# Optimization experiments

Hardware: AMD Instinct MI355X
Metric: run time of the kernel (lower is better)

Reference implementation:

```python
import jax, jax.numpy as jnp
import numpy as np

N_NODES = 50000
N_EDGES = 800000
D = 128
NEG_SLOPE = 0.2
L2_EPS = 1e-12  # torch F.normalize eps


def setup_inputs() -> dict:
    key = jax.random.key(0)
    k1, k2, k3, k4, k5 = jax.random.split(key, 5)
    node_fts = jax.random.normal(k1, (N_NODES, D), dtype=jnp.float32)
    edges = jax.random.randint(k2, (2, N_EDGES), 0, N_NODES, dtype=jnp.int32)
    edge_fts = jax.random.normal(k3, (N_EDGES, 1), dtype=jnp.float32)
    # xavier-ish init for linear weights (stored as [out, in], matching nn.Linear)
    scale = 1.414 * np.sqrt(2.0 / (D + D))
    W_self = jax.random.normal(k4, (D, D), dtype=jnp.float32) * scale
    W_neigh = jax.random.normal(k5, (D, D), dtype=jnp.float32) * scale
    return {"node_fts": node_fts, "edges": edges, "edge_fts": edge_fts,
            "W_self": W_self, "W_neigh": W_neigh}


def reference(node_fts, edges, edge_fts, W_self, W_neigh):
    n = node_fts.shape[0]
    dst_idx = edges[0]  # segment ids (aggregation targets)
    src_idx = edges[1]  # gather ids (neighbor features)

    # self transform: [N, D]
    src_node_fts = node_fts @ W_self.T

    # gather neighbor feats along edges: [E, D]
    gathered = node_fts[src_idx]

    # scatter-mean into destination nodes
    seg_sum = jax.ops.segment_sum(gathered, dst_idx, num_segments=n)  # [N, D]
    cnt = jax.ops.segment_sum(jnp.ones((gathered.shape[0], 1), dtype=node_fts.dtype),
                              dst_idx, num_segments=n)                # [N, 1]
    neigh_mean = seg_sum / jnp.maximum(cnt, 1.0)

    # linear + LeakyReLU(0.2) on aggregated neighbors
    neigh_final = jax.nn.leaky_relu(neigh_mean @ W_neigh.T, NEG_SLOPE)

    # update: sum + LeakyReLU(0.2)
    updated = jax.nn.leaky_relu(src_node_fts + neigh_final, NEG_SLOPE)

    # L2 normalize per row (torch F.normalize semantics)
    norm = jnp.linalg.norm(updated, axis=1, keepdims=True)
    return updated / jnp.maximum(norm, L2_EPS)
```

## Files before the change

kernel.cpp:

```cpp
#include <hip/hip_runtime.h>
#include <hip/hip_bf16.h>

#define N_NODES 50000
#define N_EDGES 800000
#define D 128
#define NEG 0.2f

#define NB 200
#define EPB 4000
#define NPAIR 12500
#define NCH 8
#define ROWS_PER_CH 25

#define MFMA_BLOCKS 768
#define NTILES 3125
#define COLA_BLOCKS 391
#define FILL_SLICES 1600
#define FILL_EPS 500

typedef __attribute__((ext_vector_type(8))) short bf16x8;
typedef __attribute__((ext_vector_type(4))) float f32x4;

__device__ __forceinline__ float bflo(unsigned int u) {
    return __uint_as_float(u << 16);
}
__device__ __forceinline__ float bfhi(unsigned int u) {
    return __uint_as_float(u & 0xffff0000u);
}

__global__ __launch_bounds__(256) void hist_convert_kernel(
    const int* __restrict__ dst_idx,
    unsigned int* __restrict__ bh,
    unsigned char* __restrict__ rank8,
    const float4* __restrict__ ws4, const float4* __restrict__ wn4,
    ushort4* __restrict__ wb4) {
    __shared__ unsigned int lh[NPAIR];
    const int tid = threadIdx.x, b = blockIdx.x;
    if (b < NB) {
        for (int i = tid; i < NPAIR; i += 256) lh[i] = 0u;
        __syncthreads();
        const int e0 = b * EPB;
        for (int i = tid; i < EPB; i += 256) {
            int d = dst_idx[e0 + i];
            int sh = (d & 3) * 8;
            unsigned int old = atomicAdd(&lh[d >> 2], 1u << sh);
            rank8[e0 + i] = (unsigned char)((old >> sh) & 0xffu);
        }
        __syncthreads();
        for (int i = tid; i < NPAIR; i += 256) bh[(size_t)b * NPAIR + i] = lh[i];
    } else {
        int i = (b - NB) * 256 + tid;
        const int NW = D * D / 4;
        if (i < 2 * NW) {
            float4 v = (i < NW) ? ws4[i] : wn4[i - NW];
            ushort4 o;
            __hip_bfloat16 h;
            h = __float2bfloat16(v.x); o.x = reinterpret_cast<unsigned short&>(h);
            h = __float2bfloat16(v.y); o.y = reinterpret_cast<unsigned short&>(h);
            h = __float2bfloat16(v.z); o.z = reinterpret_cast<unsigned short&>(h);
            h = __float2bfloat16(v.w); o.w = reinterpret_cast<unsigned short&>(h);
            wb4[i] = o;
        }
    }
}

__global__ __launch_bounds__(256) void mfma_colA_kernel(
    const float* __restrict__ x, const ushort* __restrict__ wb,
    unsigned int* __restrict__ sb32, unsigned int* __restrict__ zb32,
    const unsigned int* __restrict__ bh, unsigned int* __restrict__ csum) {
    __shared__ ushort tile[2][16][132];
    if (blockIdx.x < MFMA_BLOCKS) {
        const int lane = threadIdx.x & 63;
        const int wv = threadIdx.x >> 6;
        const int lm = lane & 15;
        const int lk = (lane >> 4) * 8;
        const int dr = (lane >> 4) * 4;

        bf16x8 b[4][4];
#pragma unroll
        for (int t4 = 0; t4 < 4; ++t4) {
            const int nt = wv * 4 + t4;
#pragma unroll
            for (int kc = 0; kc < 4; ++kc)
                b[t4][kc] = *(const bf16x8*)(wb + (nt * 16 + lm) * D + kc * 32 + lk);
        }

        for (int t = blockIdx.x; t < NTILES; t += MFMA_BLOCKS) {
            const int m0 = t * 16;

            bf16x8 a[4];
#pragma unroll
            for (int kc = 0; kc < 4; ++kc) {
                const float* src = x + (long)(m0 + lm) * D + kc * 32 + lk;
                float4 f0 = *(const float4*)(src);
                float4 f1 = *(const float4*)(src + 4);
                bf16x8 af;
                __hip_bfloat16 h;
                h = __float2bfloat16(f0.x); af[0] = reinterpret_cast<short&>(h);
                h = __float2bfloat16(f0.y); af[1] = reinterpret_cast<short&>(h);
                h = __float2bfloat16(f0.z); af[2] = reinterpret_cast<short&>(h);
                h = __float2bfloat16(f0.w); af[3] = reinterpret_cast<short&>(h);
                h = __float2bfloat16(f1.x); af[4] = reinterpret_cast<short&>(h);
                h = __float2bfloat16(f1.y); af[5] = reinterpret_cast<short&>(h);
                h = __float2bfloat16(f1.z); af[6] = reinterpret_cast<short&>(h);
                h = __float2bfloat16(f1.w); af[7] = reinterpret_cast<short&>(h);
                a[kc] = af;
            }

#pragma unroll
            for (int t4 = 0; t4 < 4; ++t4) {
                const int nt = wv * 4 + t4;
                f32x4 acc = {0.f, 0.f, 0.f, 0.f};
#pragma unroll
                for (int kc = 0; kc < 4; ++kc)
                    acc = __builtin_amdgcn_mfma_f32_16x16x32_bf16(a[kc], b[t4][kc], acc, 0, 0, 0);
                ushort (*tptr)[132] = (nt < 8) ? tile[0] : tile[1];
                const int col = (nt & 7) * 16 + lm;
#pragma unroll
                for (int r = 0; r < 4; ++r) {
                    __hip_bfloat16 h = __float2bfloat16(acc[r]);
                    tptr[dr + r][col] = reinterpret_cast<unsigned short&>(h);
                }
            }
            __syncthreads();
            const unsigned int* ts32 = (const unsigned int*)tile[0];
            const unsigned int* tz32 = (const unsigned int*)tile[1];
#pragma unroll
            for (int q = 0; q < 4; ++q) {
                const int r16 = wv * 4 + q;
                sb32[(m0 + r16) * 64 + lane] = ts32[r16 * 66 + lane];
                zb32[(m0 + r16) * 64 + lane] = tz32[r16 * 66 + lane];
            }
            __syncthreads();
        }
    } else {
        int gid = (blockIdx.x - MFMA_BLOCKS) * 256 + threadIdx.x;
        if (gid >= NCH * NPAIR) return;
        int c = gid / NPAIR;
        int i = gid - c * NPAIR;
        const unsigned int* col = bh + (size_t)(c * ROWS_PER_CH) * NPAIR + i;
        unsigned int s = 0u;
#pragma unroll
        for (int r = 0; r < ROWS_PER_CH; ++r) s += col[(size_t)r * NPAIR];
        csum[c * NPAIR + i] = s;
    }
}

__global__ __launch_bounds__(1024) void colscanb_scan_kernel(
    unsigned int* __restrict__ bh, const unsigned int* __restrict__ csum,
    int* __restrict__ offs) {
    const int tid = threadIdx.x;
    if (blockIdx.x < 98) {
        int gid = blockIdx.x * 1024 + tid;
        if (gid >= NCH * NPAIR) return;
        int c = gid / NPAIR;
        int i = gid - c * NPAIR;
        unsigned int run = 0u;
        for (int cc = 0; cc < c; ++cc) run += csum[cc * NPAIR + i];
        unsigned int* col = bh + (size_t)(c * ROWS_PER_CH) * NPAIR + i;
#pragma unroll
        for (int r = 0; r < ROWS_PER_CH; ++r) {
            unsigned int v = col[(size_t)r * NPAIR];
            col[(size_t)r * NPAIR] = run;
            run += v;
        }
        return;
    }
    __shared__ int wsum[16];
    __shared__ int carry_s;
    const int lane = tid & 63, wv = tid >> 6;
    if (tid == 0) { carry_s = 0; offs[N_NODES] = N_EDGES; }
    __syncthreads();
    for (int base = 0; base < NPAIR; base += 4096) {
        int i0 = base + tid * 4;
        unsigned int p0 = 0, p1 = 0, p2 = 0, p3 = 0;
#pragma unroll
        for (int j = 0; j < 4; ++j) {
            int qi = i0 + j;
            if (qi < NPAIR) {
                unsigned int s = 0;
#pragma unroll
                for (int c = 0; c < NCH; ++c) s += csum[c * NPAIR + qi];
                if (j == 0) p0 = s; else if (j == 1) p1 = s;
                else if (j == 2) p2 = s; else p3 = s;
            }
        }
        int q0 = (int)((p0 & 0xffu) + ((p0 >> 8) & 0xffu) + ((p0 >> 16) & 0xffu) + (p0 >> 24));
        int q1 = (int)((p1 & 0xffu) + ((p1 >> 8) & 0xffu) + ((p1 >> 16) & 0xffu) + (p1 >> 24));
        int q2 = (int)((p2 & 0xffu) + ((p2 >> 8) & 0xffu) + ((p2 >> 16) & 0xffu) + (p2 >> 24));
        int q3 = (int)((p3 & 0xffu) + ((p3 >> 8) & 0xffu) + ((p3 >> 16) & 0xffu) + (p3 >> 24));
        int tsum = q0 + q1 + q2 + q3;
        int xs = tsum;
#pragma unroll
        for (int off = 1; off < 64; off <<= 1) {
            int y = __shfl_up(xs, off);
            if (lane >= off) xs += y;
        }
        if (lane == 63) wsum[wv] = xs;
        __syncthreads();
        if (wv == 0 && lane < 16) {
            int s = wsum[lane];
#pragma unroll
            for (int off = 1; off < 16; off <<= 1) {
                int y = __shfl_up(s, off);
                if (lane >= off) s += y;
            }
            wsum[lane] = s;
        }
        __syncthreads();
        int waveoff = (wv == 0) ? 0 : wsum[wv - 1];
        int excl = carry_s + waveoff + xs - tsum;
        unsigned int pk[4] = {p0, p1, p2, p3};
        int qs[4] = {q0, q1, q2, q3};
        int qbase = excl;
#pragma unroll
        for (int j = 0; j < 4; ++j) {
            int qi = i0 + j;
            if (qi < NPAIR) {
                unsigned int p = pk[j];
                int d0 = (int)(p & 0xffu), d1 = (int)((p >> 8) & 0xffu);
                int d2 = (int)((p >> 16) & 0xffu);
                int4 o; o.x = qbase; o.y = o.x + d0; o.z = o.y + d1; o.w = o.z + d2;
                *(int4*)(offs + 4 * qi) = o;
            }
            qbase += qs[j];
        }
        int total = wsum[15];
        __syncthreads();
        if (tid == 0) carry_s += total;
        __syncthreads();
    }
}

__global__ __launch_bounds__(256) void fill_kernel(
    const int* __restrict__ dst_idx, const int* __restrict__ src_idx,
    const unsigned char* __restrict__ rank8,
    const unsigned char* __restrict__ bprefix,
    const int* __restrict__ offs, unsigned short* __restrict__ adj) {
    const int e0 = blockIdx.x * FILL_EPS;
    const int b = e0 / EPB;
    const unsigned char* bp = bprefix + (size_t)b * N_NODES;
    for (int i = threadIdx.x; i < FILL_EPS; i += 256) {
        int e = e0 + i;
        int d = dst_idx[e];
        int pos = offs[d] + (int)bp[d] + (int)rank8[e];
        adj[pos] = (unsigned short)src_idx[e];
    }
}

__global__ __launch_bounds__(256) void gather_final_kernel(
    const uint4* __restrict__ zb4, const uint4* __restrict__ sb4,
    const int* __restrict__ offs,
    const unsigned short* __restrict__ adj, float4* __restrict__ out4) {
    int wid = (int)((blockIdx.x * (long)blockDim.x + threadIdx.x) >> 6);
    int lane = threadIdx.x & 63;
    if (wid >= N_NODES) return;
    const int c = lane & 15, g = lane >> 4;
    int base = offs[wid];
    int len = offs[wid + 1] - base;

    float a0 = 0.f, a1 = 0.f, a2 = 0.f, a3 = 0.f;
    float a4 = 0.f, a5 = 0.f, a6 = 0.f, a7 = 0.f;

    int k = 0;
    for (; k + 8 <= len; k += 8) {
        unsigned int sA = adj[base + k + g];
        unsigned int sB = adj[base + k + 4 + g];
        uint4 vA = zb4[sA * 16u + c];
        uint4 vB = zb4[sB * 16u + c];
        a0 += bflo(vA.x); a1 += bfhi(vA.x);
        a2 += bflo(vA.y); a3 += bfhi(vA.y);
        a4 += bflo(vA.z); a5 += bfhi(vA.z);
        a6 += bflo(vA.w); a7 += bfhi(vA.w);
        a0 += bflo(vB.x); a1 += bfhi(vB.x);
        a2 += bflo(vB.y); a3 += bfhi(vB.y);
        a4 += bflo(vB.z); a5 += bfhi(vB.z);
        a6 += bflo(vB.w); a7 += bfhi(vB.w);
    }
    if (k + 4 <= len) {
        unsigned int sA = adj[base + k + g];
        uint4 vA = zb4[sA * 16u + c];
        a0 += bflo(vA.x); a1 += bfhi(vA.x);
        a2 += bflo(vA.y); a3 += bfhi(vA.y);
        a4 += bflo(vA.z); a5 += bfhi(vA.z);
        a6 += bflo(vA.w); a7 += bfhi(vA.w);
        k += 4;
    }
    int rem = len - k;
    if (g < rem) {
        unsigned int sA = adj[base + k + g];
        uint4 vA = zb4[sA * 16u + c];
        a0 += bflo(vA.x); a1 += bfhi(vA.x);
        a2 += bflo(vA.y); a3 += bfhi(vA.y);
        a4 += bflo(vA.z); a5 += bfhi(vA.z);
        a6 += bflo(vA.w); a7 += bfhi(vA.w);
    }

    a0 += __shfl_xor(a0, 16); a1 += __shfl_xor(a1, 16);
    a2 += __shfl_xor(a2, 16); a3 += __shfl_xor(a3, 16);
    a4 += __shfl_xor(a4, 16); a5 += __shfl_xor(a5, 16);
    a6 += __shfl_xor(a6, 16); a7 += __shfl_xor(a7, 16);
    a0 += __shfl_xor(a0, 32); a1 += __shfl_xor(a1, 32);
    a2 += __shfl_xor(a2, 32); a3 += __shfl_xor(a3, 32);
    a4 += __shfl_xor(a4, 32); a5 += __shfl_xor(a5, 32);
    a6 += __shfl_xor(a6, 32); a7 += __shfl_xor(a7, 32);

    float inv = 1.0f / fmaxf((float)len, 1.0f);
    float m0 = a0 * inv, m1 = a1 * inv, m2 = a2 * inv, m3 = a3 * inv;
    float m4 = a4 * inv, m5 = a5 * inv, m6 = a6 * inv, m7 = a7 * inv;
    m0 = m0 > 0.f ? m0 : NEG * m0; m1 = m1 > 0.f ? m1 : NEG * m1;
    m2 = m2 > 0.f ? m2 : NEG * m2; m3 = m3 > 0.f ? m3 : NEG * m3;
    m4 = m4 > 0.f ? m4 : NEG * m4; m5 = m5 > 0.f ? m5 : NEG * m5;
    m6 = m6 > 0.f ? m6 : NEG * m6; m7 = m7 > 0.f ? m7 : NEG * m7;

    uint4 sv = sb4[(unsigned int)wid * 16u + c];
    float u0 = bflo(sv.x) + m0, u1 = bfhi(sv.x) + m1;
    float u2 = bflo(sv.y) + m2, u3 = bfhi(sv.y) + m3;
    float u4 = bflo(sv.z) + m4, u5 = bfhi(sv.z) + m5;
    float u6 = bflo(sv.w) + m6, u7 = bfhi(sv.w) + m7;
    u0 = u0 > 0.f ? u0 : NEG * u0; u1 = u1 > 0.f ? u1 : NEG * u1;
    u2 = u2 > 0.f ? u2 : NEG * u2; u3 = u3 > 0.f ? u3 : NEG * u3;
    u4 = u4 > 0.f ? u4 : NEG * u4; u5 = u5 > 0.f ? u5 : NEG * u5;
    u6 = u6 > 0.f ? u6 : NEG * u6; u7 = u7 > 0.f ? u7 : NEG * u7;

    float ss = u0 * u0 + u1 * u1 + u2 * u2 + u3 * u3 +
               u4 * u4 + u5 * u5 + u6 * u6 + u7 * u7;
    ss += __shfl_xor(ss, 1);
    ss += __shfl_xor(ss, 2);
    ss += __shfl_xor(ss, 4);
    ss += __shfl_xor(ss, 8);
    float r = 1.0f / fmaxf(sqrtf(ss), 1e-12f);

    if (lane < 16) {
        float4 o0; o0.x = u0 * r; o0.y = u1 * r; o0.z = u2 * r; o0.w = u3 * r;
        float4 o1; o1.x = u4 * r; o1.y = u5 * r; o1.z = u6 * r; o1.w = u7 * r;
        out4[(unsigned int)wid * 32u + c * 2u] = o0;
        out4[(unsigned int)wid * 32u + c * 2u + 1u] = o1;
    }
}

extern "C" void kernel_launch(void* const* d_in, const int* in_sizes, int n_in,
                              void* d_out, int out_size, void* d_ws, size_t ws_size,
                              hipStream_t stream) {
    const float* node_fts = (const float*)d_in[0];
    const int* edges = (const int*)d_in[1];
    const float* W_self = (const float*)d_in[3];
    const float* W_neigh = (const float*)d_in[4];

    const int* dst_idx = edges;
    const int* src_idx = edges + N_EDGES;

    unsigned short* zb = (unsigned short*)d_ws;
    unsigned short* sb = zb + (size_t)N_NODES * D;
    unsigned short* wb = sb + (size_t)N_NODES * D;
    int* offs = (int*)(wb + 256 * 128);
    unsigned short* adj = (unsigned short*)(offs + N_NODES + 1);
    unsigned int* bh = (unsigned int*)(adj + N_EDGES);
    unsigned char* rank8 = (unsigned char*)(bh + (size_t)NB * NPAIR);
    unsigned int* csum = (unsigned int*)(rank8 + N_EDGES);

    hist_convert_kernel<<<NB + 32, 256, 0, stream>>>(
        dst_idx, bh, rank8,
        (const float4*)W_self, (const float4*)W_neigh, (ushort4*)wb);

    mfma_colA_kernel<<<MFMA_BLOCKS + COLA_BLOCKS, 256, 0, stream>>>(
        node_fts, wb, (unsigned int*)sb, (unsigned int*)zb, bh, csum);

    colscanb_scan_kernel<<<99, 1024, 0, stream>>>(bh, csum, offs);

    fill_kernel<<<FILL_SLICES, 256, 0, stream>>>(
        dst_idx, src_idx, rank8, (const unsigned char*)bh, offs, adj);

    int gb = (N_NODES * 64 + 255) / 256;
    gather_final_kernel<<<gb, 256, 0, stream>>>(
        (const uint4*)zb, (const uint4*)sb, offs, adj, (float4*)d_out);
}
```

Baseline: 106.3 us.

## Fuse weight conversion and MFMA transform into histogram kernel, split colA out

The histogram blocks and the MFMA dense-transform blocks now run in one launch. MFMA blocks convert the fp32 weights to bf16 in registers directly, so the separate bf16 weight buffer is gone. The column-sum pass moves into its own small kernel because it depends on the histogram results. This lets the transform overlap the histogram phase instead of running after it. In exchange, the kernel reserves the larger 50KB shared histogram for every block, which may lower occupancy for the MFMA blocks, and each MFMA block reloads the weights as fp32.

```diff
diff --git a/kernel.cpp b/kernel.cpp
--- a/kernel.cpp
+++ b/kernel.cpp
@@ -28,15 +28,31 @@
     return __uint_as_float(u & 0xffff0000u);
 }
 
-__global__ __launch_bounds__(256) void hist_convert_kernel(
+__device__ __forceinline__ bf16x8 cvt8(const float4& f0, const float4& f1) {
+    bf16x8 af;
+    __hip_bfloat16 h;
+    h = __float2bfloat16(f0.x); af[0] = reinterpret_cast<short&>(h);
+    h = __float2bfloat16(f0.y); af[1] = reinterpret_cast<short&>(h);
+    h = __float2bfloat16(f0.z); af[2] = reinterpret_cast<short&>(h);
+    h = __float2bfloat16(f0.w); af[3] = reinterpret_cast<short&>(h);
+    h = __float2bfloat16(f1.x); af[4] = reinterpret_cast<short&>(h);
+    h = __float2bfloat16(f1.y); af[5] = reinterpret_cast<short&>(h);
+    h = __float2bfloat16(f1.z); af[6] = reinterpret_cast<short&>(h);
+    h = __float2bfloat16(f1.w); af[7] = reinterpret_cast<short&>(h);
+    return af;
+}
+
+__global__ __launch_bounds__(256) void hist_mfma_kernel(
     const int* __restrict__ dst_idx,
     unsigned int* __restrict__ bh,
     unsigned char* __restrict__ rank8,
-    const float4* __restrict__ ws4, const float4* __restrict__ wn4,
-    ushort4* __restrict__ wb4) {
-    __shared__ unsigned int lh[NPAIR];
+    const float* __restrict__ Ws, const float* __restrict__ Wn,
+    const float* __restrict__ x,
+    unsigned int* __restrict__ sb32, unsigned int* __restrict__ zb32) {
+    __shared__ unsigned int smem[NPAIR];
     const int tid = threadIdx.x, b = blockIdx.x;
     if (b < NB) {
+        unsigned int* lh = smem;
         for (int i = tid; i < NPAIR; i += 256) lh[i] = 0u;
         __syncthreads();
         const int e0 = b * EPB;
@@ -49,43 +65,30 @@
         __syncthreads();
         for (int i = tid; i < NPAIR; i += 256) bh[(size_t)b * NPAIR + i] = lh[i];
     } else {
-        int i = (b - NB) * 256 + tid;
-        const int NW = D * D / 4;
-        if (i < 2 * NW) {
-            float4 v = (i < NW) ? ws4[i] : wn4[i - NW];
-            ushort4 o;
-            __hip_bfloat16 h;
-            h = __float2bfloat16(v.x); o.x = reinterpret_cast<unsigned short&>(h);
-            h = __float2bfloat16(v.y); o.y = reinterpret_cast<unsigned short&>(h);
-            h = __float2bfloat16(v.z); o.z = reinterpret_cast<unsigned short&>(h);
-            h = __float2bfloat16(v.w); o.w = reinterpret_cast<unsigned short&>(h);
-            wb4[i] = o;
-        }
-    }
-}
-
-__global__ __launch_bounds__(256) void mfma_colA_kernel(
-    const float* __restrict__ x, const ushort* __restrict__ wb,
-    unsigned int* __restrict__ sb32, unsigned int* __restrict__ zb32,
-    const unsigned int* __restrict__ bh, unsigned int* __restrict__ csum) {
-    __shared__ ushort tile[2][16][132];
-    if (blockIdx.x < MFMA_BLOCKS) {
         const int lane = threadIdx.x & 63;
         const int wv = threadIdx.x >> 6;
         const int lm = lane & 15;
         const int lk = (lane >> 4) * 8;
         const int dr = (lane >> 4) * 4;
-
-        bf16x8 b[4][4];
+        ushort (*tile0)[132] = (ushort (*)[132])smem;
+        ushort (*tile1)[132] = ((ushort (*)[132])smem) + 16;
+
+        bf16x8 bfr[4][4];
 #pragma unroll
         for (int t4 = 0; t4 < 4; ++t4) {
             const int nt = wv * 4 + t4;
-#pragma unroll
-            for (int kc = 0; kc < 4; ++kc)
-                b[t4][kc] = *(const bf16x8*)(wb + (nt * 16 + lm) * D + kc * 32 + lk);
-        }
-
-        for (int t = blockIdx.x; t < NTILES; t += MFMA_BLOCKS) {
+            const float* wrow = (wv < 2)
+                ? (Ws + (size_t)(nt * 16 + lm) * D)
+                : (Wn + (size_t)((nt - 8) * 16 + lm) * D);
+#pragma unroll
+            for (int kc = 0; kc < 4; ++kc) {
+                float4 f0 = *(const float4*)(wrow + kc * 32 + lk);
+                float4 f1 = *(const float4*)(wrow + kc * 32 + lk + 4);
+                bfr[t4][kc] = cvt8(f0, f1);
+            }
+        }
+
+        for (int t = b - NB; t < NTILES; t += MFMA_BLOCKS) {
             const int m0 = t * 16;
 
             bf16x8 a[4];
@@ -94,17 +97,7 @@
                 const float* src = x + (long)(m0 + lm) * D + kc * 32 + lk;
                 float4 f0 = *(const float4*)(src);
                 float4 f1 = *(const float4*)(src + 4);
-                bf16x8 af;
-                __hip_bfloat16 h;
-                h = __float2bfloat16(f0.x); af[0] = reinterpret_cast<short&>(h);
-                h = __float2bfloat16(f0.y); af[1] = reinterpret_cast<short&>(h);
-                h = __float2bfloat16(f0.z); af[2] = reinterpret_cast<short&>(h);
-                h = __float2bfloat16(f0.w); af[3] = reinterpret_cast<short&>(h);
-                h = __float2bfloat16(f1.x); af[4] = reinterpret_cast<short&>(h);
-                h = __float2bfloat16(f1.y); af[5] = reinterpret_cast<short&>(h);
-                h = __float2bfloat16(f1.z); af[6] = reinterpret_cast<short&>(h);
-                h = __float2bfloat16(f1.w); af[7] = reinterpret_cast<short&>(h);
-                a[kc] = af;
+                a[kc] = cvt8(f0, f1);
             }
 
 #pragma unroll
@@ -113,8 +106,8 @@
                 f32x4 acc = {0.f, 0.f, 0.f, 0.f};
 #pragma unroll
                 for (int kc = 0; kc < 4; ++kc)
-                    acc = __builtin_amdgcn_mfma_f32_16x16x32_bf16(a[kc], b[t4][kc], acc, 0, 0, 0);
-                ushort (*tptr)[132] = (nt < 8) ? tile[0] : tile[1];
+                    acc = __builtin_amdgcn_mfma_f32_16x16x32_bf16(a[kc], bfr[t4][kc], acc, 0, 0, 0);
+                ushort (*tptr)[132] = (nt < 8) ? tile0 : tile1;
                 const int col = (nt & 7) * 16 + lm;
 #pragma unroll
                 for (int r = 0; r < 4; ++r) {
@@ -123,8 +116,8 @@
                 }
             }
             __syncthreads();
-            const unsigned int* ts32 = (const unsigned int*)tile[0];
-            const unsigned int* tz32 = (const unsigned int*)tile[1];
+            const unsigned int* ts32 = (const unsigned int*)tile0;
+            const unsigned int* tz32 = (const unsigned int*)tile1;
 #pragma unroll
             for (int q = 0; q < 4; ++q) {
                 const int r16 = wv * 4 + q;
@@ -133,17 +126,20 @@
             }
             __syncthreads();
         }
-    } else {
-        int gid = (blockIdx.x - MFMA_BLOCKS) * 256 + threadIdx.x;
-        if (gid >= NCH * NPAIR) return;
-        int c = gid / NPAIR;
-        int i = gid - c * NPAIR;
-        const unsigned int* col = bh + (size_t)(c * ROWS_PER_CH) * NPAIR + i;
-        unsigned int s = 0u;
-#pragma unroll
-        for (int r = 0; r < ROWS_PER_CH; ++r) s += col[(size_t)r * NPAIR];
-        csum[c * NPAIR + i] = s;
-    }
+    }
+}
+
+__global__ __launch_bounds__(256) void colA_kernel(
+    const unsigned int* __restrict__ bh, unsigned int* __restrict__ csum) {
+    int gid = blockIdx.x * 256 + threadIdx.x;
+    if (gid >= NCH * NPAIR) return;
+    int c = gid / NPAIR;
+    int i = gid - c * NPAIR;
+    const unsigned int* col = bh + (size_t)(c * ROWS_PER_CH) * NPAIR + i;
+    unsigned int s = 0u;
+#pragma unroll
+    for (int r = 0; r < ROWS_PER_CH; ++r) s += col[(size_t)r * NPAIR];
+    csum[c * NPAIR + i] = s;
 }
 
 __global__ __launch_bounds__(1024) void colscanb_scan_kernel(
@@ -352,19 +348,17 @@
 
     unsigned short* zb = (unsigned short*)d_ws;
     unsigned short* sb = zb + (size_t)N_NODES * D;
-    unsigned short* wb = sb + (size_t)N_NODES * D;
-    int* offs = (int*)(wb + 256 * 128);
+    int* offs = (int*)(sb + (size_t)N_NODES * D);
     unsigned short* adj = (unsigned short*)(offs + N_NODES + 1);
     unsigned int* bh = (unsigned int*)(adj + N_EDGES);
     unsigned char* rank8 = (unsigned char*)(bh + (size_t)NB * NPAIR);
     unsigned int* csum = (unsigned int*)(rank8 + N_EDGES);
 
-    hist_convert_kernel<<<NB + 32, 256, 0, stream>>>(
-        dst_idx, bh, rank8,
-        (const float4*)W_self, (const float4*)W_neigh, (ushort4*)wb);
-
-    mfma_colA_kernel<<<MFMA_BLOCKS + COLA_BLOCKS, 256, 0, stream>>>(
-        node_fts, wb, (unsigned int*)sb, (unsigned int*)zb, bh, csum);
+    hist_mfma_kernel<<<NB + MFMA_BLOCKS, 256, 0, stream>>>(
+        dst_idx, bh, rank8, W_self, W_neigh, node_fts,
+        (unsigned int*)sb, (unsigned int*)zb);
+
+    colA_kernel<<<COLA_BLOCKS, 256, 0, stream>>>(bh, csum);
 
     colscanb_scan_kernel<<<99, 1024, 0, stream>>>(bh, csum, offs);
 
```

New measurement: 109.4 us. 1.03x slower.
